# Performance work log

Hardware: AMD Instinct MI355X
Metric: run time of the kernel (lower is better)

The kernel has to match this reference:

```python
import jax, jax.numpy as jnp
import numpy as np

B, T, I = 64, 256, 512   # batch, timesteps, input_size
S, D, H = 256, 1024, 1024  # stoch_size, deter_size, dec_hidden_size


def _p(key, shape, scale=0.05):
    return scale * jax.random.normal(key, shape, dtype=jnp.float32)


def gru_cell(x, h, W_ih, W_hh, b_ih, b_hh):
    # torch nn.GRU single-step cell
    gi = x @ W_ih.T + b_ih            # [B, 3D]
    gh = h @ W_hh.T + b_hh            # [B, 3D]
    i_r, i_z, i_n = jnp.split(gi, 3, axis=-1)
    h_r, h_z, h_n = jnp.split(gh, 3, axis=-1)
    r = jax.nn.sigmoid(i_r + h_r)
    z = jax.nn.sigmoid(i_z + h_z)
    n = jnp.tanh(i_n + r * h_n)
    return (1.0 - z) * n + z * h


def setup_inputs() -> dict:
    key = jax.random.key(0)
    ks = jax.random.split(key, 16)
    x = jax.random.normal(ks[0], (B, T, I), dtype=jnp.float32)
    noise = jax.random.normal(ks[1], (T, B, S), dtype=jnp.float32)  # posterior reparam noise per step
    # GRU params (input = stoch z, hidden = deter)
    W_ih = _p(ks[2], (3 * D, S)); W_hh = _p(ks[3], (3 * D, D))
    b_ih = jnp.zeros((3 * D,), jnp.float32); b_hh = jnp.zeros((3 * D,), jnp.float32)
    # posterior heads: input = concat(x_t, deter)
    Wm = _p(ks[4], (S, I + D)); bm = jnp.zeros((S,), jnp.float32)
    Wv = _p(ks[5], (S, I + D)); bv = jnp.zeros((S,), jnp.float32)
    # decoder MLP: (S+D) -> H -> H -> H -> I  (dec_num_layers=3, ELU)
    dec_W0 = _p(ks[6], (H, S + D)); dec_b0 = jnp.zeros((H,), jnp.float32)
    dec_W1 = _p(ks[7], (H, H));     dec_b1 = jnp.zeros((H,), jnp.float32)
    dec_W2 = _p(ks[8], (H, H));     dec_b2 = jnp.zeros((H,), jnp.float32)
    dec_W3 = _p(ks[9], (I, H));     dec_b3 = jnp.zeros((I,), jnp.float32)
    return dict(x=x, noise=noise, W_ih=W_ih, W_hh=W_hh, b_ih=b_ih, b_hh=b_hh,
                Wm=Wm, bm=bm, Wv=Wv, bv=bv,
                dec_W0=dec_W0, dec_b0=dec_b0, dec_W1=dec_W1, dec_b1=dec_b1,
                dec_W2=dec_W2, dec_b2=dec_b2, dec_W3=dec_W3, dec_b3=dec_b3)


def reference(x, noise, W_ih, W_hh, b_ih, b_hh, Wm, bm, Wv, bv,
              dec_W0, dec_b0, dec_W1, dec_b1, dec_W2, dec_b2, dec_W3, dec_b3):
    xs = jnp.transpose(x, (1, 0, 2))  # [T, B, I]

    def step(carry, inp):
        h, z_in = carry
        xt, nt = inp
        h = gru_cell(z_in, h, W_ih, W_hh, b_ih, b_hh)        # deter state [B, D]
        post_in = jnp.concatenate([xt, h], axis=-1)          # [B, I+D]
        mean = post_in @ Wm.T + bm
        std = jnp.exp(0.5 * (post_in @ Wv.T + bv))
        z = nt * std + mean                                   # reparameterized posterior sample
        return (h, z), (h, z)

    h0 = jnp.zeros((B, D), jnp.float32)
    z0 = jnp.zeros((B, S), jnp.float32)
    _, (deter, stoch) = jax.lax.scan(step, (h0, z0), (xs, noise))  # [T, B, D], [T, B, S]

    deter = jnp.transpose(deter, (1, 0, 2))  # [B, T, D]
    stoch = jnp.transpose(stoch, (1, 0, 2))  # [B, T, S]
    rssm = jnp.concatenate([deter, stoch], axis=-1)  # [B, T, D+S]

    a = jax.nn.elu(rssm @ dec_W0.T + dec_b0)
    a = jax.nn.elu(a @ dec_W1.T + dec_b1)
    a = jax.nn.elu(a @ dec_W2.T + dec_b2)
    dist_inputs = a @ dec_W3.T + dec_b3      # [B, T, I]
    x_delta_hat = dist_inputs[:, :-1, :]     # [B, T-1, I]

    x_hat = jnp.concatenate([x[:, :1, :], x[:, :-1, :] + x_delta_hat], axis=1)
    return (x_delta_hat, x_hat)
```

## Files before the change

### kernel.cpp

```cpp
#include <hip/hip_runtime.h>
#include <hip/hip_bf16.h>
#include <string.h>

typedef __bf16 bf16x8 __attribute__((ext_vector_type(8)));
typedef float f32x4 __attribute__((ext_vector_type(4)));

#define MFMA16(a, b, c) __builtin_amdgcn_mfma_f32_16x16x32_bf16((a), (b), (c), 0, 0, 0)

#define BB 64
#define TT 256
#define II 512
#define SS 256
#define DD 1024
#define HH 1024

#define OFF_A ((size_t)0)
#define OFF_Z ((size_t)33554432)
#define OFF_HB ((size_t)41943040)
#define OFF_ZB ((size_t)42205184)
#define OFF_CNT ((size_t)42237952)

#define DO_XM ((size_t)35651584)
#define DO_XV ((size_t)44040192)
#define DO_WB0 ((size_t)52428800)
#define DO_WB1 ((size_t)55050240)
#define DO_WB2 ((size_t)57147392)
#define OUTD_ELEMS 8355840

#define NGRU 128
#define NPST 16

__device__ __forceinline__ float fsig(float x) { return 1.f / (1.f + __expf(-x)); }
__device__ __forceinline__ float ftanh(float x) {
  float ax = __builtin_fabsf(x);
  float e = __expf(-2.f * ax);
  float r = (1.f - e) / (1.f + e);
  return __builtin_copysignf(r, x);
}

__device__ __forceinline__ bf16x8 ld8f(const float* p) {
  float4 a = *(const float4*)p;
  float4 b = *(const float4*)(p + 4);
  bf16x8 r;
  r[0] = (__bf16)a.x; r[1] = (__bf16)a.y; r[2] = (__bf16)a.z; r[3] = (__bf16)a.w;
  r[4] = (__bf16)b.x; r[5] = (__bf16)b.y; r[6] = (__bf16)b.z; r[7] = (__bf16)b.w;
  return r;
}

__device__ __forceinline__ void wait_flags(int* flags, int n, int target, bool acq) {
  if ((int)threadIdx.x < n) {
    while (__hip_atomic_load(flags + threadIdx.x, __ATOMIC_RELAXED, __HIP_MEMORY_SCOPE_AGENT) <
           target)
      __builtin_amdgcn_s_sleep(1);
  }
  __syncthreads();
  if (acq) {
    if (threadIdx.x == 0)
      (void)__hip_atomic_load(flags, __ATOMIC_ACQUIRE, __HIP_MEMORY_SCOPE_AGENT);
    __syncthreads();
  }
}
__device__ __forceinline__ void st2(__bf16* p, float v) {
  __bf16 hv = (__bf16)v;
  unsigned short ub;
  __builtin_memcpy(&ub, &hv, 2);
  __hip_atomic_store((unsigned short*)p, ub, __ATOMIC_RELAXED, __HIP_MEMORY_SCOPE_AGENT);
}

__global__ __launch_bounds__(256) void k_xmv(const float* __restrict__ x,
                                             const float* __restrict__ Wm,
                                             const float* __restrict__ Wv,
                                             const float* __restrict__ Wd0,
                                             const float* __restrict__ Wd1,
                                             const float* __restrict__ Wd2,
                                             char* __restrict__ doutc, char* __restrict__ ws) {
  if (blockIdx.x == 0 && blockIdx.y == 0) {
    int* cnt = (int*)(ws + OFF_CNT);
    cnt[threadIdx.x] = 0;
    cnt[threadIdx.x + 256] = 0;
  }
  {
    size_t lin = (size_t)blockIdx.y * 256 + blockIdx.x;
    size_t g = (lin * 256 + threadIdx.x) * 8;
    if (g < 3407872) {
      const float* src;
      __bf16* dst;
      if (g < 1310720) {
        src = Wd0 + g;
        dst = (__bf16*)(doutc + DO_WB0) + g;
      } else if (g < 2359296) {
        src = Wd1 + (g - 1310720);
        dst = (__bf16*)(doutc + DO_WB1) + (g - 1310720);
      } else {
        src = Wd2 + (g - 2359296);
        dst = (__bf16*)(doutc + DO_WB2) + (g - 2359296);
      }
      *(bf16x8*)dst = ld8f(src);
    }
  }
  __bf16* xm = (__bf16*)(doutc + DO_XM);
  __bf16* xv = (__bf16*)(doutc + DO_XV);

  int m0 = blockIdx.x * 64, n0 = blockIdx.y * 64;
  int tid = threadIdx.x, lane = tid & 63, wv = tid >> 6;
  int n15 = lane & 15, q8 = (lane >> 4) * 8;

  int row = m0 + wv * 16 + n15;
  int t = row >> 6, b = row & 63;
  const float* arow = x + ((size_t)(b * TT + t)) * II + q8;

  const float* brow[4];
#pragma unroll
  for (int j = 0; j < 4; ++j) {
    int c = n0 + j * 16 + n15;
    brow[j] = ((c < SS) ? (Wm + (size_t)c * (II + DD)) : (Wv + (size_t)(c - SS) * (II + DD))) + q8;
  }
  f32x4 acc[4] = {};
#pragma unroll 4
  for (int k = 0; k < II; k += 32) {
    bf16x8 a = ld8f(arow + k);
#pragma unroll
    for (int j = 0; j < 4; ++j) acc[j] = MFMA16(a, ld8f(brow[j] + k), acc[j]);
  }
  int mb = m0 + wv * 16 + (lane >> 4) * 4;
#pragma unroll
  for (int j = 0; j < 4; ++j) {
    int c = n0 + j * 16 + n15;
    __bf16* dst = (c < SS) ? (xm + c) : (xv + (c - SS));
#pragma unroll
    for (int r = 0; r < 4; ++r) dst[(size_t)(mb + r) * SS] = (__bf16)acc[j][r];
  }
}

__global__ __launch_bounds__(256, 1) void k_scan(
    const float* __restrict__ Wih, const float* __restrict__ Whh,
    const float* __restrict__ bih, const float* __restrict__ bhh,
    const float* __restrict__ Wm, const float* __restrict__ bm,
    const float* __restrict__ Wv, const float* __restrict__ bv,
    const float* __restrict__ noise, char* __restrict__ ws, char* __restrict__ doutc) {
  __shared__ __bf16 smem[32768];

  __bf16* hbL[2] = {(__bf16*)(ws + OFF_HB), (__bf16*)(ws + OFF_HB) + (size_t)BB * DD};
  __bf16* zb = (__bf16*)(ws + OFF_ZB);
  __bf16* z_all = (__bf16*)(ws + OFF_Z);
  __bf16* h_all = (__bf16*)doutc;
  const __bf16* xm = (const __bf16*)(doutc + DO_XM);
  const __bf16* xv = (const __bf16*)(doutc + DO_XV);
  int* hflag = (int*)(ws + OFF_CNT);
  int* zflag = hflag + 256;

  int blk = blockIdx.x, tid = threadIdx.x, lane = tid & 63, wv = tid >> 6;
  int n15 = lane & 15, q = lane >> 4, q8 = q * 8, q4 = q * 4;
  const int rb = wv * 16 + n15;

  if (blk < NGRU) {
    int c0 = blk * 8;
    int col8 = n15 & 7;
    int swq = (q + ((col8 >> 1) & 3)) & 3;
    for (int u = tid; u < 3072; u += 256) {
      int qq = u & 3, col = (u >> 2) & 7, kk = (u >> 5) & 31, g = u >> 10;
      int sq = (qq + ((col >> 1) & 3)) & 3;
      *(bf16x8*)(smem + ((((g * 32 + kk) * 8 + col) * 4) + sq) * 8) =
          ld8f(Whh + ((size_t)(g * DD + c0 + col)) * DD + kk * 32 + qq * 8);
    }
    for (int u = tid; u < 768; u += 256) {
      int qq = u & 3, col = (u >> 2) & 7, kk = (u >> 5) & 7, g = u >> 8;
      int sq = (qq + ((col >> 1) & 3)) & 3;
      *(bf16x8*)(smem + 24576 + ((((g * 8 + kk) * 8 + col) * 4) + sq) * 8) =
          ld8f(Wih + ((size_t)(g * DD + c0 + col)) * SS + kk * 32 + qq * 8);
    }
    __syncthreads();

    int ccb = c0 + col8;
    float brs = bih[ccb] + bhh[ccb];
    float bzs = bih[DD + ccb] + bhh[DD + ccb];
    float bin = bih[2 * DD + ccb];
    float bhn = bhh[2 * DD + ccb];
    f32x4 hcarry = {};
    int mb = wv * 16 + q4;

    for (int t = 0; t < TT; ++t) {
      f32x4 accr = {}, accz = {}, acchn = {}, accin = {};
      if (t > 0) {
        wait_flags(hflag, NGRU, t, true);
        const __bf16* hp = hbL[t & 1] + (size_t)rb * DD + q8;
        bf16x8 hA[32];
#pragma unroll
        for (int kk = 0; kk < 32; ++kk) hA[kk] = *(const bf16x8*)(hp + kk * 32);
#pragma unroll
        for (int kk = 0; kk < 32; ++kk) {
          const __bf16* wb = smem + ((size_t)kk * 8 + col8) * 32 + swq * 8;
          accr = MFMA16(hA[kk], *(const bf16x8*)(wb), accr);
          accz = MFMA16(hA[kk], *(const bf16x8*)(wb + 8192), accz);
          acchn = MFMA16(hA[kk], *(const bf16x8*)(wb + 16384), acchn);
        }
        wait_flags(zflag, NPST, t, false);
        const __bf16* zp = zb + (size_t)rb * SS + q8;
        bf16x8 zA[8];
#pragma unroll
        for (int kk = 0; kk < 8; ++kk) zA[kk] = *(const bf16x8*)(zp + kk * 32);
#pragma unroll
        for (int kk = 0; kk < 8; ++kk) {
          const __bf16* wb = smem + 24576 + ((size_t)kk * 8 + col8) * 32 + swq * 8;
          accr = MFMA16(zA[kk], *(const bf16x8*)(wb), accr);
          accz = MFMA16(zA[kk], *(const bf16x8*)(wb + 2048), accz);
          accin = MFMA16(zA[kk], *(const bf16x8*)(wb + 4096), accin);
        }
      }
      __bf16* hw = hbL[(t + 1) & 1];
      __bf16* hall_t = h_all + (size_t)t * BB * DD;
#pragma unroll
      for (int r = 0; r < 4; ++r) {
        int mm = mb + r;
        float rg = fsig(accr[r] + brs);
        float zg = fsig(accz[r] + bzs);
        float ng = ftanh(accin[r] + bin + rg * (acchn[r] + bhn));
        float hn = (1.f - zg) * ng + zg * hcarry[r];
        hcarry[r] = hn;
        if (n15 < 8) {
          st2(hw + (size_t)mm * DD + ccb, hn);
          hall_t[(size_t)mm * DD + ccb] = (__bf16)hn;
        }
      }
      asm volatile("s_waitcnt vmcnt(0)" ::: "memory");
      __syncthreads();
      if (tid == 0)
        __hip_atomic_store(hflag + blk, t + 1, __ATOMIC_RELAXED, __HIP_MEMORY_SCOPE_AGENT);
    }
  } else {
    int p = blk - NGRU, cp0 = p * 16;
    int swq = (q + ((n15 >> 1) & 3)) & 3;
    for (int u = tid; u < 4096; u += 256) {
      int qq = u & 3, col = (u >> 2) & 15, kk = (u >> 6) & 31, mv = u >> 11;
      int sq = (qq + ((col >> 1) & 3)) & 3;
      const float* src = (mv ? Wv : Wm) + ((size_t)(cp0 + col)) * (II + DD) + II + kk * 32 + qq * 8;
      *(bf16x8*)(smem + ((((mv * 32 + kk) * 16 + col) * 4) + sq) * 8) = ld8f(src);
    }
    __syncthreads();

    int c2 = cp0 + n15;
    float bmv = bm[c2], bvv = bv[c2];
    int mb = wv * 16 + q4;

    for (int t = 0; t < TT; ++t) {
      wait_flags(hflag, NGRU, t + 1, true);
      const __bf16* hp = hbL[(t + 1) & 1] + (size_t)rb * DD + q8;
      bf16x8 hA[32];
#pragma unroll
      for (int kk = 0; kk < 32; ++kk) hA[kk] = *(const bf16x8*)(hp + kk * 32);
      f32x4 am = {}, av = {};
#pragma unroll
      for (int kk = 0; kk < 32; ++kk) {
        const __bf16* wb = smem + ((size_t)kk * 16 + n15) * 32 + swq * 8;
        am = MFMA16(hA[kk], *(const bf16x8*)(wb), am);
        av = MFMA16(hA[kk], *(const bf16x8*)(wb + 16384), av);
      }
#pragma unroll
      for (int r = 0; r < 4; ++r) {
        int mm = mb + r;
        size_t gidx = ((size_t)t * BB + mm) * SS + c2;
        float mean = am[r] + bmv + (float)xm[gidx];
        float vr = av[r] + bvv + (float)xv[gidx];
        float sd = __expf(0.5f * vr);
        float zt = noise[gidx] * sd + mean;
        st2(zb + (size_t)mm * SS + c2, zt);
        z_all[gidx] = (__bf16)zt;
      }
      asm volatile("s_waitcnt vmcnt(0)" ::: "memory");
      __syncthreads();
      if (tid == 0)
        __hip_atomic_store(zflag + p, t + 1, __ATOMIC_RELAXED, __HIP_MEMORY_SCOPE_AGENT);
    }
  }
}

__global__ __launch_bounds__(256, 2) void k_dec0(const char* __restrict__ doutc,
                                                 const char* __restrict__ ws,
                                                 const float* __restrict__ b0,
                                                 __bf16* __restrict__ C) {
  const __bf16* h_all = (const __bf16*)doutc;
  const __bf16* z_all = (const __bf16*)(ws + OFF_Z);
  const __bf16* W0b = (const __bf16*)(doutc + DO_WB0);
  int m0 = blockIdx.x * 128, n0 = blockIdx.y * 128;
  int tid = threadIdx.x, lane = tid & 63, w = tid >> 6;
  int wm = w >> 1, wn = w & 1;
  int n15 = lane & 15, q8 = (lane >> 4) * 8, q4 = (lane >> 4) * 4;

  const __bf16* hrow[4];
  const __bf16* zrow[4];
  const __bf16* brow[4];
#pragma unroll
  for (int i = 0; i < 4; ++i) {
    int row = m0 + wm * 64 + i * 16 + n15;
    int b = row >> 8, tq = row & 255;
    hrow[i] = h_all + ((size_t)tq * BB + b) * DD + q8;
    zrow[i] = z_all + ((size_t)tq * BB + b) * SS + q8;
  }
#pragma unroll
  for (int j = 0; j < 4; ++j)
    brow[j] = W0b + (size_t)(n0 + wn * 64 + j * 16 + n15) * (DD + SS) + q8;

  f32x4 acc[4][4] = {};
  for (int k = 0; k < DD + SS; k += 32) {
    bf16x8 af[4], bfv[4];
#pragma unroll
    for (int i = 0; i < 4; ++i)
      af[i] = (k < DD) ? *(const bf16x8*)(hrow[i] + k) : *(const bf16x8*)(zrow[i] + k - DD);
#pragma unroll
    for (int j = 0; j < 4; ++j) bfv[j] = *(const bf16x8*)(brow[j] + k);
#pragma unroll
    for (int i = 0; i < 4; ++i)
#pragma unroll
      for (int j = 0; j < 4; ++j) acc[i][j] = MFMA16(af[i], bfv[j], acc[i][j]);
  }
#pragma unroll
  for (int i = 0; i < 4; ++i) {
    int mr = m0 + wm * 64 + i * 16 + q4;
#pragma unroll
    for (int j = 0; j < 4; ++j) {
      int c = n0 + wn * 64 + j * 16 + n15;
      float bb = b0[c];
#pragma unroll
      for (int r = 0; r < 4; ++r) {
        float v = acc[i][j][r] + bb;
        v = v > 0.f ? v : (__expf(v) - 1.f);
        C[(size_t)(mr + r) * HH + c] = (__bf16)v;
      }
    }
  }
}

__global__ __launch_bounds__(256, 2) void k_dec_mid(const __bf16* __restrict__ A,
                                                    const __bf16* __restrict__ W,
                                                    const float* __restrict__ bias,
                                                    __bf16* __restrict__ C) {
  int m0 = blockIdx.x * 128, n0 = blockIdx.y * 128;
  int tid = threadIdx.x, lane = tid & 63, w = tid >> 6;
  int wm = w >> 1, wn = w & 1;
  int n15 = lane & 15, q8 = (lane >> 4) * 8, q4 = (lane >> 4) * 4;

  const __bf16* arow[4];
  const __bf16* brow[4];
#pragma unroll
  for (int i = 0; i < 4; ++i) arow[i] = A + (size_t)(m0 + wm * 64 + i * 16 + n15) * DD + q8;
#pragma unroll
  for (int j = 0; j < 4; ++j) brow[j] = W + (size_t)(n0 + wn * 64 + j * 16 + n15) * DD + q8;

  f32x4 acc[4][4] = {};
  for (int k = 0; k < DD; k += 32) {
    bf16x8 af[4], bfv[4];
#pragma unroll
    for (int i = 0; i < 4; ++i) af[i] = *(const bf16x8*)(arow[i] + k);
#pragma unroll
    for (int j = 0; j < 4; ++j) bfv[j] = *(const bf16x8*)(brow[j] + k);
#pragma unroll
    for (int i = 0; i < 4; ++i)
#pragma unroll
      for (int j = 0; j < 4; ++j) acc[i][j] = MFMA16(af[i], bfv[j], acc[i][j]);
  }
#pragma unroll
  for (int i = 0; i < 4; ++i) {
    int mr = m0 + wm * 64 + i * 16 + q4;
#pragma unroll
    for (int j = 0; j < 4; ++j) {
      int c = n0 + wn * 64 + j * 16 + n15;
      float bb = bias[c];
#pragma unroll
      for (int r = 0; r < 4; ++r) {
        float v = acc[i][j][r] + bb;
        v = v > 0.f ? v : (__expf(v) - 1.f);
        C[(size_t)(mr + r) * HH + c] = (__bf16)v;
      }
    }
  }
}

__global__ __launch_bounds__(256, 2) void k_dec3(const __bf16* __restrict__ A,
                                                 const float* __restrict__ W3,
                                                 const float* __restrict__ b3,
                                                 const float* __restrict__ x,
                                                 float* __restrict__ outd,
                                                 float* __restrict__ outh) {
  int m0 = blockIdx.x * 128, n0 = blockIdx.y * 128;
  int tid = threadIdx.x, lane = tid & 63, w = tid >> 6;
  int wm = w >> 1, wn = w & 1;
  int n15 = lane & 15, q8 = (lane >> 4) * 8, q4 = (lane >> 4) * 4;

  const __bf16* arow[4];
  const float* brow[4];
#pragma unroll
  for (int i = 0; i < 4; ++i) arow[i] = A + (size_t)(m0 + wm * 64 + i * 16 + n15) * HH + q8;
#pragma unroll
  for (int j = 0; j < 4; ++j) brow[j] = W3 + (size_t)(n0 + wn * 64 + j * 16 + n15) * HH + q8;

  f32x4 acc[4][4] = {};
  for (int k = 0; k < HH; k += 32) {
    bf16x8 af[4], bfv[4];
#pragma unroll
    for (int i = 0; i < 4; ++i) af[i] = *(const bf16x8*)(arow[i] + k);
#pragma unroll
    for (int j = 0; j < 4; ++j) bfv[j] = ld8f(brow[j] + k);
#pragma unroll
    for (int i = 0; i < 4; ++i)
#pragma unroll
      for (int j = 0; j < 4; ++j) acc[i][j] = MFMA16(af[i], bfv[j], acc[i][j]);
  }
#pragma unroll
  for (int i = 0; i < 4; ++i) {
    int mr = m0 + wm * 64 + i * 16 + q4;
#pragma unroll
    for (int j = 0; j < 4; ++j) {
      int c = n0 + wn * 64 + j * 16 + n15;
      float b3v = b3[c];
#pragma unroll
      for (int r = 0; r < 4; ++r) {
        int mm = mr + r;
        int b = mm >> 8, tq = mm & 255;
        float dv = acc[i][j][r] + b3v;
        if (tq < 255) {
          outd[((size_t)b * 255 + tq) * II + c] = dv;
          outh[((size_t)b * TT + tq + 1) * II + c] = x[((size_t)b * TT + tq) * II + c] + dv;
        }
        if (tq == 0) outh[((size_t)b * TT) * II + c] = x[((size_t)b * TT) * II + c];
      }
    }
  }
}

extern "C" void kernel_launch(void* const* d_in, const int* in_sizes, int n_in,
                              void* d_out, int out_size, void* d_ws, size_t ws_size,
                              hipStream_t stream) {
  const float* x = (const float*)d_in[0];
  const float* noise = (const float*)d_in[1];
  const float* W_ih = (const float*)d_in[2];
  const float* W_hh = (const float*)d_in[3];
  const float* b_ih = (const float*)d_in[4];
  const float* b_hh = (const float*)d_in[5];
  const float* Wm = (const float*)d_in[6];
  const float* bm = (const float*)d_in[7];
  const float* Wv = (const float*)d_in[8];
  const float* bv = (const float*)d_in[9];
  const float* dW0 = (const float*)d_in[10];
  const float* db0 = (const float*)d_in[11];
  const float* dW1 = (const float*)d_in[12];
  const float* db1 = (const float*)d_in[13];
  const float* dW2 = (const float*)d_in[14];
  const float* db2 = (const float*)d_in[15];
  const float* dW3 = (const float*)d_in[16];
  const float* db3 = (const float*)d_in[17];

  char* ws = (char*)d_ws;
  char* doutc = (char*)d_out;
  __bf16* a0 = (__bf16*)(ws + OFF_A);
  __bf16* a1 = (__bf16*)doutc;
  __bf16* a2 = (__bf16*)(ws + OFF_A);

  k_xmv<<<dim3(256, 8), 256, 0, stream>>>(x, Wm, Wv, dW0, dW1, dW2, doutc, ws);

  k_scan<<<NGRU + NPST, 256, 0, stream>>>(W_ih, W_hh, b_ih, b_hh, Wm, bm, Wv, bv, noise, ws,
                                          doutc);

  k_dec0<<<dim3(128, 8), 256, 0, stream>>>(doutc, ws, db0, a0);
  k_dec_mid<<<dim3(128, 8), 256, 0, stream>>>(a0, (const __bf16*)(doutc + DO_WB1), db1, a1);
  k_dec_mid<<<dim3(128, 8), 256, 0, stream>>>(a1, (const __bf16*)(doutc + DO_WB2), db2, a2);
  k_dec3<<<dim3(128, 4), 256, 0, stream>>>(a2, dW3, db3, x, (float*)doutc,
                                           (float*)doutc + OUTD_ELEMS);
}
```

Before: 4.897 ms.

## Drop acquire fences in flag waits and defer history stores past signal

The inter-block flag wait no longer performs an acquire load plus an extra barrier. Instead, the shared h/z buffers are read with relaxed agent-scope atomic 64-bit loads so they bypass stale cache lines. The h_all/z_all history stores are moved after the flag signal and made nontemporal, which takes them off the critical path before each step's s_waitcnt and handoff. This shortens the per-timestep serial latency of the recurrent loop. The risk is memory-ordering correctness if relaxed loads do not observe the producer's data without an acquire.

```diff
diff --git a/kernel.cpp b/kernel.cpp
--- a/kernel.cpp
+++ b/kernel.cpp
@@ -47,18 +47,22 @@
   return r;
 }
 
-__device__ __forceinline__ void wait_flags(int* flags, int n, int target, bool acq) {
+__device__ __forceinline__ bf16x8 ld8c(const __bf16* p) {
+  const unsigned long long* q = (const unsigned long long*)p;
+  unsigned long long u0 = __hip_atomic_load(q, __ATOMIC_RELAXED, __HIP_MEMORY_SCOPE_AGENT);
+  unsigned long long u1 = __hip_atomic_load(q + 1, __ATOMIC_RELAXED, __HIP_MEMORY_SCOPE_AGENT);
+  union { unsigned long long u[2]; bf16x8 v; } r;
+  r.u[0] = u0; r.u[1] = u1;
+  return r.v;
+}
+
+__device__ __forceinline__ void wait_flags(int* flags, int n, int target) {
   if ((int)threadIdx.x < n) {
     while (__hip_atomic_load(flags + threadIdx.x, __ATOMIC_RELAXED, __HIP_MEMORY_SCOPE_AGENT) <
            target)
       __builtin_amdgcn_s_sleep(1);
   }
   __syncthreads();
-  if (acq) {
-    if (threadIdx.x == 0)
-      (void)__hip_atomic_load(flags, __ATOMIC_ACQUIRE, __HIP_MEMORY_SCOPE_AGENT);
-    __syncthreads();
-  }
 }
 __device__ __forceinline__ void st2(__bf16* p, float v) {
   __bf16 hv = (__bf16)v;
@@ -182,11 +186,11 @@
     for (int t = 0; t < TT; ++t) {
       f32x4 accr = {}, accz = {}, acchn = {}, accin = {};
       if (t > 0) {
-        wait_flags(hflag, NGRU, t, true);
+        wait_flags(hflag, NGRU, t);
         const __bf16* hp = hbL[t & 1] + (size_t)rb * DD + q8;
         bf16x8 hA[32];
 #pragma unroll
-        for (int kk = 0; kk < 32; ++kk) hA[kk] = *(const bf16x8*)(hp + kk * 32);
+        for (int kk = 0; kk < 32; ++kk) hA[kk] = ld8c(hp + kk * 32);
 #pragma unroll
         for (int kk = 0; kk < 32; ++kk) {
           const __bf16* wb = smem + ((size_t)kk * 8 + col8) * 32 + swq * 8;
@@ -194,11 +198,11 @@
           accz = MFMA16(hA[kk], *(const bf16x8*)(wb + 8192), accz);
           acchn = MFMA16(hA[kk], *(const bf16x8*)(wb + 16384), acchn);
         }
-        wait_flags(zflag, NPST, t, false);
+        wait_flags(zflag, NPST, t);
         const __bf16* zp = zb + (size_t)rb * SS + q8;
         bf16x8 zA[8];
 #pragma unroll
-        for (int kk = 0; kk < 8; ++kk) zA[kk] = *(const bf16x8*)(zp + kk * 32);
+        for (int kk = 0; kk < 8; ++kk) zA[kk] = ld8c(zp + kk * 32);
 #pragma unroll
         for (int kk = 0; kk < 8; ++kk) {
           const __bf16* wb = smem + 24576 + ((size_t)kk * 8 + col8) * 32 + swq * 8;
@@ -217,15 +221,17 @@
         float ng = ftanh(accin[r] + bin + rg * (acchn[r] + bhn));
         float hn = (1.f - zg) * ng + zg * hcarry[r];
         hcarry[r] = hn;
-        if (n15 < 8) {
-          st2(hw + (size_t)mm * DD + ccb, hn);
-          hall_t[(size_t)mm * DD + ccb] = (__bf16)hn;
-        }
+        if (n15 < 8) st2(hw + (size_t)mm * DD + ccb, hn);
       }
       asm volatile("s_waitcnt vmcnt(0)" ::: "memory");
       __syncthreads();
       if (tid == 0)
         __hip_atomic_store(hflag + blk, t + 1, __ATOMIC_RELAXED, __HIP_MEMORY_SCOPE_AGENT);
+      if (n15 < 8) {
+#pragma unroll
+        for (int r = 0; r < 4; ++r)
+          __builtin_nontemporal_store((__bf16)hcarry[r], hall_t + (size_t)(mb + r) * DD + ccb);
+      }
     }
   } else {
     int p = blk - NGRU, cp0 = p * 16;
@@ -243,11 +249,11 @@
     int mb = wv * 16 + q4;
 
     for (int t = 0; t < TT; ++t) {
-      wait_flags(hflag, NGRU, t + 1, true);
+      wait_flags(hflag, NGRU, t + 1);
       const __bf16* hp = hbL[(t + 1) & 1] + (size_t)rb * DD + q8;
       bf16x8 hA[32];
 #pragma unroll
-      for (int kk = 0; kk < 32; ++kk) hA[kk] = *(const bf16x8*)(hp + kk * 32);
+      for (int kk = 0; kk < 32; ++kk) hA[kk] = ld8c(hp + kk * 32);
       f32x4 am = {}, av = {};
 #pragma unroll
       for (int kk = 0; kk < 32; ++kk) {
@@ -255,6 +261,7 @@
         am = MFMA16(hA[kk], *(const bf16x8*)(wb), am);
         av = MFMA16(hA[kk], *(const bf16x8*)(wb + 16384), av);
       }
+      f32x4 zs;
 #pragma unroll
       for (int r = 0; r < 4; ++r) {
         int mm = mb + r;
@@ -263,13 +270,17 @@
         float vr = av[r] + bvv + (float)xv[gidx];
         float sd = __expf(0.5f * vr);
         float zt = noise[gidx] * sd + mean;
+        zs[r] = zt;
         st2(zb + (size_t)mm * SS + c2, zt);
-        z_all[gidx] = (__bf16)zt;
       }
       asm volatile("s_waitcnt vmcnt(0)" ::: "memory");
       __syncthreads();
       if (tid == 0)
         __hip_atomic_store(zflag + p, t + 1, __ATOMIC_RELAXED, __HIP_MEMORY_SCOPE_AGENT);
+#pragma unroll
+      for (int r = 0; r < 4; ++r)
+        __builtin_nontemporal_store((__bf16)zs[r],
+                                    z_all + ((size_t)t * BB + mb + r) * SS + c2);
     }
   }
 }
```

New measurement: 5.385 ms. 1.1x slower.

## Halve scan workgroups with wider column tiles and move history stores off critical path

Applied to the files above, without the earlier changes.

The persistent scan kernel now uses 64 GRU blocks owning 16 hidden columns each and 8 posterior blocks owning 32 stochastic columns each, so LDS weight staging doubles to 128KB. All 16 MFMA output lanes now do useful work instead of half being masked. Fewer blocks means fewer flags to poll at each cross-block barrier every timestep. The h/z history writes are moved after the flag release and use nontemporal stores, taking them off the critical path. The cost is more MFMA work per block per step, so per-block latency rises.

```diff
diff --git a/kernel.cpp b/kernel.cpp
--- a/kernel.cpp
+++ b/kernel.cpp
@@ -27,8 +27,8 @@
 #define DO_WB2 ((size_t)57147392)
 #define OUTD_ELEMS 8355840
 
-#define NGRU 128
-#define NPST 16
+#define NGRU 64
+#define NPST 8
 
 __device__ __forceinline__ float fsig(float x) { return 1.f / (1.f + __expf(-x)); }
 __device__ __forceinline__ float ftanh(float x) {
@@ -138,7 +138,7 @@
     const float* __restrict__ Wm, const float* __restrict__ bm,
     const float* __restrict__ Wv, const float* __restrict__ bv,
     const float* __restrict__ noise, char* __restrict__ ws, char* __restrict__ doutc) {
-  __shared__ __bf16 smem[32768];
+  __shared__ __bf16 smem[65536];
 
   __bf16* hbL[2] = {(__bf16*)(ws + OFF_HB), (__bf16*)(ws + OFF_HB) + (size_t)BB * DD};
   __bf16* zb = (__bf16*)(ws + OFF_ZB);
@@ -152,26 +152,25 @@
   int blk = blockIdx.x, tid = threadIdx.x, lane = tid & 63, wv = tid >> 6;
   int n15 = lane & 15, q = lane >> 4, q8 = q * 8, q4 = q * 4;
   const int rb = wv * 16 + n15;
+  int swq = (q + ((n15 >> 1) & 3)) & 3;
 
   if (blk < NGRU) {
-    int c0 = blk * 8;
-    int col8 = n15 & 7;
-    int swq = (q + ((col8 >> 1) & 3)) & 3;
-    for (int u = tid; u < 3072; u += 256) {
-      int qq = u & 3, col = (u >> 2) & 7, kk = (u >> 5) & 31, g = u >> 10;
+    int c0 = blk * 16;
+    for (int u = tid; u < 6144; u += 256) {
+      int qq = u & 3, col = (u >> 2) & 15, kk = (u >> 6) & 31, g = u >> 11;
       int sq = (qq + ((col >> 1) & 3)) & 3;
-      *(bf16x8*)(smem + ((((g * 32 + kk) * 8 + col) * 4) + sq) * 8) =
+      *(bf16x8*)(smem + ((((g * 32 + kk) * 16 + col) * 4) + sq) * 8) =
           ld8f(Whh + ((size_t)(g * DD + c0 + col)) * DD + kk * 32 + qq * 8);
     }
-    for (int u = tid; u < 768; u += 256) {
-      int qq = u & 3, col = (u >> 2) & 7, kk = (u >> 5) & 7, g = u >> 8;
+    for (int u = tid; u < 1536; u += 256) {
+      int qq = u & 3, col = (u >> 2) & 15, kk = (u >> 6) & 7, g = u >> 9;
       int sq = (qq + ((col >> 1) & 3)) & 3;
-      *(bf16x8*)(smem + 24576 + ((((g * 8 + kk) * 8 + col) * 4) + sq) * 8) =
+      *(bf16x8*)(smem + 49152 + ((((g * 8 + kk) * 16 + col) * 4) + sq) * 8) =
           ld8f(Wih + ((size_t)(g * DD + c0 + col)) * SS + kk * 32 + qq * 8);
     }
     __syncthreads();
 
-    int ccb = c0 + col8;
+    int ccb = c0 + n15;
     float brs = bih[ccb] + bhh[ccb];
     float bzs = bih[DD + ccb] + bhh[DD + ccb];
     float bin = bih[2 * DD + ccb];
@@ -189,10 +188,10 @@
         for (int kk = 0; kk < 32; ++kk) hA[kk] = *(const bf16x8*)(hp + kk * 32);
 #pragma unroll
         for (int kk = 0; kk < 32; ++kk) {
-          const __bf16* wb = smem + ((size_t)kk * 8 + col8) * 32 + swq * 8;
+          const __bf16* wb = smem + ((size_t)kk * 16 + n15) * 32 + swq * 8;
           accr = MFMA16(hA[kk], *(const bf16x8*)(wb), accr);
-          accz = MFMA16(hA[kk], *(const bf16x8*)(wb + 8192), accz);
-          acchn = MFMA16(hA[kk], *(const bf16x8*)(wb + 16384), acchn);
+          accz = MFMA16(hA[kk], *(const bf16x8*)(wb + 16384), accz);
+          acchn = MFMA16(hA[kk], *(const bf16x8*)(wb + 32768), acchn);
         }
         wait_flags(zflag, NPST, t, false);
         const __bf16* zp = zb + (size_t)rb * SS + q8;
@@ -201,10 +200,10 @@
         for (int kk = 0; kk < 8; ++kk) zA[kk] = *(const bf16x8*)(zp + kk * 32);
 #pragma unroll
         for (int kk = 0; kk < 8; ++kk) {
-          const __bf16* wb = smem + 24576 + ((size_t)kk * 8 + col8) * 32 + swq * 8;
+          const __bf16* wb = smem + 49152 + ((size_t)kk * 16 + n15) * 32 + swq * 8;
           accr = MFMA16(zA[kk], *(const bf16x8*)(wb), accr);
-          accz = MFMA16(zA[kk], *(const bf16x8*)(wb + 2048), accz);
-          accin = MFMA16(zA[kk], *(const bf16x8*)(wb + 4096), accin);
+          accz = MFMA16(zA[kk], *(const bf16x8*)(wb + 4096), accz);
+          accin = MFMA16(zA[kk], *(const bf16x8*)(wb + 8192), accin);
         }
       }
       __bf16* hw = hbL[(t + 1) & 1];
@@ -217,29 +216,29 @@
         float ng = ftanh(accin[r] + bin + rg * (acchn[r] + bhn));
         float hn = (1.f - zg) * ng + zg * hcarry[r];
         hcarry[r] = hn;
-        if (n15 < 8) {
-          st2(hw + (size_t)mm * DD + ccb, hn);
-          hall_t[(size_t)mm * DD + ccb] = (__bf16)hn;
-        }
+        st2(hw + (size_t)mm * DD + ccb, hn);
       }
       asm volatile("s_waitcnt vmcnt(0)" ::: "memory");
       __syncthreads();
       if (tid == 0)
         __hip_atomic_store(hflag + blk, t + 1, __ATOMIC_RELAXED, __HIP_MEMORY_SCOPE_AGENT);
+#pragma unroll
+      for (int r = 0; r < 4; ++r)
+        __builtin_nontemporal_store((__bf16)hcarry[r], hall_t + (size_t)(mb + r) * DD + ccb);
     }
   } else {
-    int p = blk - NGRU, cp0 = p * 16;
-    int swq = (q + ((n15 >> 1) & 3)) & 3;
-    for (int u = tid; u < 4096; u += 256) {
-      int qq = u & 3, col = (u >> 2) & 15, kk = (u >> 6) & 31, mv = u >> 11;
+    int p = blk - NGRU, cp0 = p * 32;
+    for (int u = tid; u < 8192; u += 256) {
+      int qq = u & 3, col = (u >> 2) & 31, kk = (u >> 7) & 31, mv = u >> 12;
       int sq = (qq + ((col >> 1) & 3)) & 3;
       const float* src = (mv ? Wv : Wm) + ((size_t)(cp0 + col)) * (II + DD) + II + kk * 32 + qq * 8;
-      *(bf16x8*)(smem + ((((mv * 32 + kk) * 16 + col) * 4) + sq) * 8) = ld8f(src);
+      *(bf16x8*)(smem + ((((mv * 32 + kk) * 32 + col) * 4) + sq) * 8) = ld8f(src);
     }
     __syncthreads();
 
-    int c2 = cp0 + n15;
-    float bmv = bm[c2], bvv = bv[c2];
+    int c2a = cp0 + n15, c2b = cp0 + 16 + n15;
+    float bmv0 = bm[c2a], bvv0 = bv[c2a];
+    float bmv1 = bm[c2b], bvv1 = bv[c2b];
     int mb = wv * 16 + q4;
 
     for (int t = 0; t < TT; ++t) {
@@ -248,28 +247,45 @@
       bf16x8 hA[32];
 #pragma unroll
       for (int kk = 0; kk < 32; ++kk) hA[kk] = *(const bf16x8*)(hp + kk * 32);
-      f32x4 am = {}, av = {};
+      f32x4 am[2] = {}, av[2] = {};
 #pragma unroll
       for (int kk = 0; kk < 32; ++kk) {
-        const __bf16* wb = smem + ((size_t)kk * 16 + n15) * 32 + swq * 8;
-        am = MFMA16(hA[kk], *(const bf16x8*)(wb), am);
-        av = MFMA16(hA[kk], *(const bf16x8*)(wb + 16384), av);
-      }
-#pragma unroll
-      for (int r = 0; r < 4; ++r) {
-        int mm = mb + r;
-        size_t gidx = ((size_t)t * BB + mm) * SS + c2;
-        float mean = am[r] + bmv + (float)xm[gidx];
-        float vr = av[r] + bvv + (float)xv[gidx];
-        float sd = __expf(0.5f * vr);
-        float zt = noise[gidx] * sd + mean;
-        st2(zb + (size_t)mm * SS + c2, zt);
-        z_all[gidx] = (__bf16)zt;
+#pragma unroll
+        for (int jt = 0; jt < 2; ++jt) {
+          const __bf16* wb = smem + ((size_t)kk * 32 + jt * 16 + n15) * 32 + swq * 8;
+          am[jt] = MFMA16(hA[kk], *(const bf16x8*)(wb), am[jt]);
+          av[jt] = MFMA16(hA[kk], *(const bf16x8*)(wb + 32768), av[jt]);
+        }
+      }
+      f32x4 zs[2];
+#pragma unroll
+      for (int jt = 0; jt < 2; ++jt) {
+        int c2 = jt ? c2b : c2a;
+        float bmv = jt ? bmv1 : bmv0, bvv = jt ? bvv1 : bvv0;
+#pragma unroll
+        for (int r = 0; r < 4; ++r) {
+          int mm = mb + r;
+          size_t gidx = ((size_t)t * BB + mm) * SS + c2;
+          float mean = am[jt][r] + bmv + (float)xm[gidx];
+          float vr = av[jt][r] + bvv + (float)xv[gidx];
+          float sd = __expf(0.5f * vr);
+          float zt = noise[gidx] * sd + mean;
+          zs[jt][r] = zt;
+          st2(zb + (size_t)mm * SS + c2, zt);
+        }
       }
       asm volatile("s_waitcnt vmcnt(0)" ::: "memory");
       __syncthreads();
       if (tid == 0)
         __hip_atomic_store(zflag + p, t + 1, __ATOMIC_RELAXED, __HIP_MEMORY_SCOPE_AGENT);
+#pragma unroll
+      for (int jt = 0; jt < 2; ++jt) {
+        int c2 = jt ? c2b : c2a;
+#pragma unroll
+        for (int r = 0; r < 4; ++r)
+          __builtin_nontemporal_store((__bf16)zs[jt][r],
+                                      z_all + ((size_t)t * BB + mb + r) * SS + c2);
+      }
     }
   }
 }
```

After: 5.672 ms. +15.8%, slower.

## Transpose scan MFMA operands for packed 8-byte state stores and defer history writes

Applied to the files above, without the earlier changes.

The scan kernel swaps MFMA A/B operands so each lane holds four consecutive output columns of one batch row. The per-step h and z state can then go out as a single 8-byte atomic store instead of four 2-byte ones. History writes to h_all and z_all are deferred to the next step and issued as nontemporal stores overlapping the MFMA loop, so they no longer sit on the vmcnt(0) critical path before the flag release. Noise, xm and xv loads are hoisted ahead of the flag wait, and the acquire in wait_flags merges into one barrier; this touches the memory-ordering logic of the inter-block sync.

```diff
diff --git a/kernel.cpp b/kernel.cpp
--- a/kernel.cpp
+++ b/kernel.cpp
@@ -3,6 +3,7 @@
 #include <string.h>
 
 typedef __bf16 bf16x8 __attribute__((ext_vector_type(8)));
+typedef __bf16 bf16x4 __attribute__((ext_vector_type(4)));
 typedef float f32x4 __attribute__((ext_vector_type(4)));
 
 #define MFMA16(a, b, c) __builtin_amdgcn_mfma_f32_16x16x32_bf16((a), (b), (c), 0, 0, 0)
@@ -47,24 +48,25 @@
   return r;
 }
 
+__device__ __forceinline__ unsigned long long pack4(const f32x4 v) {
+  union { __bf16 h[4]; unsigned long long u; } r;
+  r.h[0] = (__bf16)v[0]; r.h[1] = (__bf16)v[1];
+  r.h[2] = (__bf16)v[2]; r.h[3] = (__bf16)v[3];
+  return r.u;
+}
+
 __device__ __forceinline__ void wait_flags(int* flags, int n, int target, bool acq) {
   if ((int)threadIdx.x < n) {
     while (__hip_atomic_load(flags + threadIdx.x, __ATOMIC_RELAXED, __HIP_MEMORY_SCOPE_AGENT) <
            target)
       __builtin_amdgcn_s_sleep(1);
   }
+  if (acq && threadIdx.x == 0)
+    (void)__hip_atomic_load(flags, __ATOMIC_ACQUIRE, __HIP_MEMORY_SCOPE_AGENT);
   __syncthreads();
-  if (acq) {
-    if (threadIdx.x == 0)
-      (void)__hip_atomic_load(flags, __ATOMIC_ACQUIRE, __HIP_MEMORY_SCOPE_AGENT);
-    __syncthreads();
-  }
-}
-__device__ __forceinline__ void st2(__bf16* p, float v) {
-  __bf16 hv = (__bf16)v;
-  unsigned short ub;
-  __builtin_memcpy(&ub, &hv, 2);
-  __hip_atomic_store((unsigned short*)p, ub, __ATOMIC_RELAXED, __HIP_MEMORY_SCOPE_AGENT);
+}
+__device__ __forceinline__ void st8(void* p, unsigned long long u) {
+  __hip_atomic_store((unsigned long long*)p, u, __ATOMIC_RELAXED, __HIP_MEMORY_SCOPE_AGENT);
 }
 
 __global__ __launch_bounds__(256) void k_xmv(const float* __restrict__ x,
@@ -150,7 +152,7 @@
   int* zflag = hflag + 256;
 
   int blk = blockIdx.x, tid = threadIdx.x, lane = tid & 63, wv = tid >> 6;
-  int n15 = lane & 15, q = lane >> 4, q8 = q * 8, q4 = q * 4;
+  int n15 = lane & 15, q = lane >> 4, q8 = q * 8;
   const int rb = wv * 16 + n15;
 
   if (blk < NGRU) {
@@ -171,13 +173,14 @@
     }
     __syncthreads();
 
-    int ccb = c0 + col8;
-    float brs = bih[ccb] + bhh[ccb];
-    float bzs = bih[DD + ccb] + bhh[DD + ccb];
-    float bin = bih[2 * DD + ccb];
-    float bhn = bhh[2 * DD + ccb];
+    int colw = c0 + (q & 1) * 4;
+    f32x4 brs = *(const f32x4*)(bih + colw);
+    brs += *(const f32x4*)(bhh + colw);
+    f32x4 bzs = *(const f32x4*)(bih + DD + colw);
+    bzs += *(const f32x4*)(bhh + DD + colw);
+    f32x4 bin4 = *(const f32x4*)(bih + 2 * DD + colw);
+    f32x4 bhn4 = *(const f32x4*)(bhh + 2 * DD + colw);
     f32x4 hcarry = {};
-    int mb = wv * 16 + q4;
 
     for (int t = 0; t < TT; ++t) {
       f32x4 accr = {}, accz = {}, acchn = {}, accin = {};
@@ -187,12 +190,16 @@
         bf16x8 hA[32];
 #pragma unroll
         for (int kk = 0; kk < 32; ++kk) hA[kk] = *(const bf16x8*)(hp + kk * 32);
+        if (q < 2)
+          __builtin_nontemporal_store(
+              pack4(hcarry),
+              (unsigned long long*)(h_all + (size_t)(t - 1) * BB * DD + (size_t)rb * DD + colw));
 #pragma unroll
         for (int kk = 0; kk < 32; ++kk) {
           const __bf16* wb = smem + ((size_t)kk * 8 + col8) * 32 + swq * 8;
-          accr = MFMA16(hA[kk], *(const bf16x8*)(wb), accr);
-          accz = MFMA16(hA[kk], *(const bf16x8*)(wb + 8192), accz);
-          acchn = MFMA16(hA[kk], *(const bf16x8*)(wb + 16384), acchn);
+          accr = MFMA16(*(const bf16x8*)(wb), hA[kk], accr);
+          accz = MFMA16(*(const bf16x8*)(wb + 8192), hA[kk], accz);
+          acchn = MFMA16(*(const bf16x8*)(wb + 16384), hA[kk], acchn);
         }
         wait_flags(zflag, NPST, t, false);
         const __bf16* zp = zb + (size_t)rb * SS + q8;
@@ -202,31 +209,29 @@
 #pragma unroll
         for (int kk = 0; kk < 8; ++kk) {
           const __bf16* wb = smem + 24576 + ((size_t)kk * 8 + col8) * 32 + swq * 8;
-          accr = MFMA16(zA[kk], *(const bf16x8*)(wb), accr);
-          accz = MFMA16(zA[kk], *(const bf16x8*)(wb + 2048), accz);
-          accin = MFMA16(zA[kk], *(const bf16x8*)(wb + 4096), accin);
+          accr = MFMA16(*(const bf16x8*)(wb), zA[kk], accr);
+          accz = MFMA16(*(const bf16x8*)(wb + 2048), zA[kk], accz);
+          accin = MFMA16(*(const bf16x8*)(wb + 4096), zA[kk], accin);
         }
       }
       __bf16* hw = hbL[(t + 1) & 1];
-      __bf16* hall_t = h_all + (size_t)t * BB * DD;
 #pragma unroll
       for (int r = 0; r < 4; ++r) {
-        int mm = mb + r;
-        float rg = fsig(accr[r] + brs);
-        float zg = fsig(accz[r] + bzs);
-        float ng = ftanh(accin[r] + bin + rg * (acchn[r] + bhn));
-        float hn = (1.f - zg) * ng + zg * hcarry[r];
-        hcarry[r] = hn;
-        if (n15 < 8) {
-          st2(hw + (size_t)mm * DD + ccb, hn);
-          hall_t[(size_t)mm * DD + ccb] = (__bf16)hn;
-        }
-      }
+        float rg = fsig(accr[r] + brs[r]);
+        float zg = fsig(accz[r] + bzs[r]);
+        float ng = ftanh(accin[r] + bin4[r] + rg * (acchn[r] + bhn4[r]));
+        hcarry[r] = (1.f - zg) * ng + zg * hcarry[r];
+      }
+      if (q < 2) st8(hw + (size_t)rb * DD + colw, pack4(hcarry));
       asm volatile("s_waitcnt vmcnt(0)" ::: "memory");
       __syncthreads();
       if (tid == 0)
         __hip_atomic_store(hflag + blk, t + 1, __ATOMIC_RELAXED, __HIP_MEMORY_SCOPE_AGENT);
     }
+    if (q < 2)
+      __builtin_nontemporal_store(
+          pack4(hcarry),
+          (unsigned long long*)(h_all + (size_t)(TT - 1) * BB * DD + (size_t)rb * DD + colw));
   } else {
     int p = blk - NGRU, cp0 = p * 16;
     int swq = (q + ((n15 >> 1) & 3)) & 3;
@@ -238,39 +243,48 @@
     }
     __syncthreads();
 
-    int c2 = cp0 + n15;
-    float bmv = bm[c2], bvv = bv[c2];
-    int mb = wv * 16 + q4;
+    int c4 = cp0 + q * 4;
+    f32x4 bmv = *(const f32x4*)(bm + c4);
+    f32x4 bvv = *(const f32x4*)(bv + c4);
+    f32x4 zsPrev = {};
 
     for (int t = 0; t < TT; ++t) {
+      size_t base = ((size_t)t * BB + rb) * SS + c4;
+      f32x4 nz = *(const f32x4*)(noise + base);
+      bf16x4 xm4 = *(const bf16x4*)(xm + base);
+      bf16x4 xv4 = *(const bf16x4*)(xv + base);
+
       wait_flags(hflag, NGRU, t + 1, true);
       const __bf16* hp = hbL[(t + 1) & 1] + (size_t)rb * DD + q8;
       bf16x8 hA[32];
 #pragma unroll
       for (int kk = 0; kk < 32; ++kk) hA[kk] = *(const bf16x8*)(hp + kk * 32);
+      if (t > 0)
+        __builtin_nontemporal_store(
+            pack4(zsPrev),
+            (unsigned long long*)(z_all + ((size_t)(t - 1) * BB + rb) * SS + c4));
       f32x4 am = {}, av = {};
 #pragma unroll
       for (int kk = 0; kk < 32; ++kk) {
         const __bf16* wb = smem + ((size_t)kk * 16 + n15) * 32 + swq * 8;
-        am = MFMA16(hA[kk], *(const bf16x8*)(wb), am);
-        av = MFMA16(hA[kk], *(const bf16x8*)(wb + 16384), av);
+        am = MFMA16(*(const bf16x8*)(wb), hA[kk], am);
+        av = MFMA16(*(const bf16x8*)(wb + 16384), hA[kk], av);
       }
 #pragma unroll
       for (int r = 0; r < 4; ++r) {
-        int mm = mb + r;
-        size_t gidx = ((size_t)t * BB + mm) * SS + c2;
-        float mean = am[r] + bmv + (float)xm[gidx];
-        float vr = av[r] + bvv + (float)xv[gidx];
+        float mean = am[r] + bmv[r] + (float)xm4[r];
+        float vr = av[r] + bvv[r] + (float)xv4[r];
         float sd = __expf(0.5f * vr);
-        float zt = noise[gidx] * sd + mean;
-        st2(zb + (size_t)mm * SS + c2, zt);
-        z_all[gidx] = (__bf16)zt;
-      }
+        zsPrev[r] = nz[r] * sd + mean;
+      }
+      st8(zb + (size_t)rb * SS + c4, pack4(zsPrev));
       asm volatile("s_waitcnt vmcnt(0)" ::: "memory");
       __syncthreads();
       if (tid == 0)
         __hip_atomic_store(zflag + p, t + 1, __ATOMIC_RELAXED, __HIP_MEMORY_SCOPE_AGENT);
     }
+    __builtin_nontemporal_store(
+        pack4(zsPrev), (unsigned long long*)(z_all + ((size_t)(TT - 1) * BB + rb) * SS + c4));
   }
 }
 
```

New measurement: 4.253 ms. 13.2% less time.
